# Kernel tuning notes

Measured on AMD Instinct MI355X. Metric: run time of the kernel, lower is better.

## Reference

```python
import jax, jax.numpy as jnp
import numpy as np
from jax import lax

B, H, W, CL, CC, CD, NH, NP = 8, 48, 48, 384, 384, 384, 12, 4
N = H * W
HD = CL // NH
SCALE = HD ** -0.5


def _pool_mat(n, out=7):
    # torch AdaptiveAvgPool2d bin edges: [floor(i*n/out), ceil((i+1)*n/out))
    M = np.zeros((out, n), np.float32)
    for i in range(out):
        s = (i * n) // out
        e = -(-((i + 1) * n) // out)
        M[i, s:e] = 1.0 / (e - s)
    return jnp.asarray(M)


def _resize_mat(out_n, in_n):
    # bilinear, align_corners=False (torch F.interpolate)
    M = np.zeros((out_n, in_n), np.float32)
    scale = in_n / out_n
    for o in range(out_n):
        src = (o + 0.5) * scale - 0.5
        src = min(max(src, 0.0), in_n - 1.0)
        i0 = int(np.floor(src))
        i1 = min(i0 + 1, in_n - 1)
        f = src - i0
        M[o, i0] += 1.0 - f
        M[o, i1] += f
    return jnp.asarray(M)


def _ln_c(x, g, b):
    # LayerNorm over channel dim of NCHW, eps=1e-6
    mu = jnp.mean(x, axis=1, keepdims=True)
    var = jnp.mean((x - mu) ** 2, axis=1, keepdims=True)
    xn = (x - mu) * lax.rsqrt(var + 1e-6)
    return xn * g[None, :, None, None] + b[None, :, None, None]


def _c1(x, w):
    # 1x1 conv, w: (out,in)
    return jnp.einsum('oc,bchw->bohw', w, x)


def _bilerp(feat, grid):
    # feat (G,C,Hs,Ws), grid (G,M,2) xy in [-1,1]; align_corners=False, zero padding
    G, C, Hs, Ws = feat.shape
    x = (grid[..., 0] + 1.0) * 0.5 * Ws - 0.5
    y = (grid[..., 1] + 1.0) * 0.5 * Hs - 0.5
    x0 = jnp.floor(x)
    y0 = jnp.floor(y)
    fx = x - x0
    fy = y - y0
    featf = feat.transpose(0, 2, 3, 1).reshape(G, Hs * Ws, C)
    x0i = x0.astype(jnp.int32)
    y0i = y0.astype(jnp.int32)

    def corner(ix, iy):
        valid = ((ix >= 0) & (ix < Ws) & (iy >= 0) & (iy < Hs)).astype(feat.dtype)
        flat = jnp.clip(iy, 0, Hs - 1) * Ws + jnp.clip(ix, 0, Ws - 1)
        g = jax.vmap(lambda f, i: f[i])(featf, flat)  # (G,M,C)
        return g * valid[..., None]

    v00 = corner(x0i, y0i)
    v01 = corner(x0i + 1, y0i)
    v10 = corner(x0i, y0i + 1)
    v11 = corner(x0i + 1, y0i + 1)
    w00 = ((1 - fx) * (1 - fy))[..., None]
    w01 = (fx * (1 - fy))[..., None]
    w10 = ((1 - fx) * fy)[..., None]
    w11 = (fx * fy)[..., None]
    return v00 * w00 + v01 * w01 + v10 * w10 + v11 * w11  # (G,M,C)


def _forward(local_feat, context_prior, deformable_x, W_q, W_k, W_v, W_pre, ln1_g, ln1_b,
             W_post, dw_w, dw_b, ln2_g, ln2_b, W_lo, b_lo, W_off, b_off,
             attention_biases, W_p, bn_g, bn_b, bn_mean, bn_var):
    q = _c1(local_feat, W_q)  # (B,CL,H,W)

    # context_offset_guide: 1x1 -> GELU -> adaptive pool 7x7 -> LN(C) -> 1x1 to 32 -> resize
    cg = jax.nn.gelu(_c1(context_prior, W_pre), approximate=False)
    Mh, Mw = _pool_mat(H), _pool_mat(W)
    pooled = jnp.einsum('oh,pw,bchw->bcop', Mh, Mw, cg)
    guide = _c1(_ln_c(pooled, ln1_g, ln1_b), W_post)  # (B,32,7,7)
    Uh, Uw = _resize_mat(H, 7), _resize_mat(W, 7)
    guide = jnp.einsum('Oh,Pw,bchw->bcOP', Uh, Uw, guide)  # (B,32,H,W)

    # local_offset_base: dwconv3x3 -> LN(C) -> GELU -> 1x1 to 32
    dw = lax.conv_general_dilated(local_feat, dw_w, (1, 1), [(1, 1), (1, 1)],
                                  dimension_numbers=('NCHW', 'OIHW', 'NCHW'),
                                  feature_group_count=CL) + dw_b[None, :, None, None]
    lo = jax.nn.gelu(_ln_c(dw, ln2_g, ln2_b), approximate=False)
    lo = _c1(lo, W_lo) + b_lo[None, :, None, None]  # (B,32,H,W)

    fused = jnp.concatenate([guide, lo], axis=1)  # (B,64,H,W)
    off = _c1(fused, W_off) + b_off[None, :, None, None]  # (B,NH*NP*2,H,W)
    off = off.transpose(0, 2, 3, 1).reshape(B, H, W, NH, NP, 2)
    offn = off / jnp.asarray([W, H], dtype=off.dtype)

    ry = (jnp.arange(H, dtype=off.dtype) + 0.5) / H
    rx = (jnp.arange(W, dtype=off.dtype) + 0.5) / W
    ref = jnp.stack([jnp.broadcast_to(rx[None, :], (H, W)),
                     jnp.broadcast_to(ry[:, None], (H, W))], axis=-1)  # (H,W,2) xy
    grid = (ref[None, :, :, None, None, :] + offn) * 2.0 - 1.0  # (B,H,W,NH,NP,2)

    gridh = grid.reshape(B, N, NH, NP, 2).transpose(0, 2, 1, 3, 4)  # (B,NH,N,NP,2)
    grid_r = gridh.reshape(B * NH, N * NP, 2)

    k = _c1(context_prior, W_k).reshape(B * NH, HD, H, W)
    v = _c1(deformable_x, W_v).reshape(B * NH, HD, H, W)
    k_s = _bilerp(k, grid_r).reshape(B, NH, N, NP, HD)
    v_s = _bilerp(v, grid_r).reshape(B, NH, N, NP, HD)

    qh = q.reshape(B, NH, HD, N).transpose(0, 1, 3, 2)  # (B,NH,N,HD)
    scores = jnp.einsum('bhnd,bhnpd->bhnp', qh, k_s) * SCALE

    # relative position bias: idx(p1,p2) = |dy|*W + |dx| (first-seen enumeration)
    px = jnp.clip(jnp.round((gridh[..., 0] + 1.0) * 0.5 * W - 0.5), 0, W - 1).astype(jnp.int32)
    py = jnp.clip(jnp.round((gridh[..., 1] + 1.0) * 0.5 * H - 0.5), 0, H - 1).astype(jnp.int32)
    n = jnp.arange(N, dtype=jnp.int32)
    qy = (n // W)[None, None, :, None]
    qx = (n % W)[None, None, :, None]
    bidx = jnp.abs(qy - py) * W + jnp.abs(qx - px)  # (B,NH,N,NP)
    bias = attention_biases[jnp.arange(NH)[None, :, None, None], bidx]

    attn = jax.nn.softmax(scores + bias, axis=-1)
    out = jnp.einsum('bhnp,bhnpd->bhnd', attn, v_s)  # (B,NH,N,HD)
    out = out.transpose(0, 1, 3, 2).reshape(B, CL, H, W)

    y = _c1(out, W_p)
    y = bn_g[None, :, None, None] * (y - bn_mean[None, :, None, None]) * \
        lax.rsqrt(bn_var[None, :, None, None] + 1e-5) + bn_b[None, :, None, None]
    return y


def setup_inputs():
    ks = jax.random.split(jax.random.key(0), 16)
    f32 = jnp.float32
    d = {
        'local_feat': jax.random.normal(ks[0], (B, CL, H, W), f32),
        'context_prior': jax.random.normal(ks[1], (B, CC, H, W), f32),
        'deformable_x': jax.random.normal(ks[2], (B, CD, H, W), f32),
        'W_q': jax.random.normal(ks[3], (CL, CL), f32) * 0.02,
        'W_k': jax.random.normal(ks[4], (CL, CC), f32) * 0.02,
        'W_v': jax.random.normal(ks[5], (CD, CD), f32) * 0.02,
        'W_pre': jax.random.normal(ks[6], (CC, CC), f32) * 0.02,
        'ln1_g': jnp.ones((CC,), f32),
        'ln1_b': jnp.zeros((CC,), f32),
        'W_post': jax.random.normal(ks[7], (32, CC), f32) * 0.02,
        'dw_w': jax.random.normal(ks[8], (CL, 1, 3, 3), f32) * 0.1,
        'dw_b': jnp.zeros((CL,), f32),
        'ln2_g': jnp.ones((CL,), f32),
        'ln2_b': jnp.zeros((CL,), f32),
        'W_lo': jax.random.normal(ks[9], (32, CL), f32) * 0.02,
        'b_lo': jnp.zeros((32,), f32),
        'W_off': jax.random.normal(ks[10], (NH * NP * 2, 64), f32) * 0.01,
        'b_off': jax.random.normal(ks[11], (NH * NP * 2,), f32) * 0.5,
        'attention_biases': jax.random.normal(ks[12], (NH, H * W), f32) * 0.02,
        'W_p': jax.random.normal(ks[13], (CL, CL), f32) * 0.02,
        'bn_g': jnp.ones((CL,), f32),
        'bn_b': jnp.zeros((CL,), f32),
        'bn_mean': jax.random.normal(ks[14], (CL,), f32) * 0.01,
        'bn_var': jax.random.uniform(ks[15], (CL,), f32, 0.5, 1.5),
    }
    return d


def reference(local_feat, context_prior, deformable_x, W_q, W_k, W_v, W_pre, ln1_g, ln1_b,
              W_post, dw_w, dw_b, ln2_g, ln2_b, W_lo, b_lo, W_off, b_off,
              attention_biases, W_p, bn_g, bn_b, bn_mean, bn_var):
    return _forward(local_feat, context_prior, deformable_x, W_q, W_k, W_v, W_pre, ln1_g,
                    ln1_b, W_post, dw_w, dw_b, ln2_g, ln2_b, W_lo, b_lo, W_off, b_off,
                    attention_biases, W_p, bn_g, bn_b, bn_mean, bn_var)
```

## Files before the change

### kernel.cpp

```cpp
#include <hip/hip_runtime.h>
#include <hip/hip_bf16.h>
#include <math.h>

#define B_ 8
#define H_ 48
#define W_ 48
#define N_ 2304
#define C_ 384
#define NH_ 12
#define NP_ 4
#define HD_ 32
#define SCALE_ 0.17677669529663687f

typedef unsigned short ushort;
typedef short bf16x8 __attribute__((ext_vector_type(8)));
typedef float f32x4 __attribute__((ext_vector_type(4)));

__device__ __forceinline__ float b2f(ushort u) {
    union { float f; unsigned i; } x; x.i = ((unsigned)u) << 16; return x.f;
}
__device__ __forceinline__ ushort f2b(float f) {
    __hip_bfloat16 h = __float2bfloat16(f);
    return *(ushort*)&h;
}
__device__ __forceinline__ float geluf(float x) {
    return 0.5f * x * (1.0f + erff(x * 0.70710678118654752440f));
}
__device__ __forceinline__ int iabs(int x) { return x < 0 ? -x : x; }

__device__ __forceinline__ void gl_lds16(const ushort* g, ushort* l) {
    __builtin_amdgcn_global_load_lds(
        (const __attribute__((address_space(1))) unsigned int*)g,
        (__attribute__((address_space(3))) unsigned int*)l, 16, 0, 0);
}

enum { EPI_NONE = 0, EPI_GELU = 1, EPI_BN = 3 };

__global__ void probe_kernel(const void* ones_ptr, int* flag) {
    if (threadIdx.x == 0 && blockIdx.x == 0)
        *flag = (*(const unsigned*)ones_ptr == 0x3F803F80u) ? 1 : 0;
}

#define PREP_MAX 24
struct PrepTab {
    const void* src[PREP_MAX];
    void*       dst[PREP_MAX];
    int         n[PREP_MAX];
    int         tobf[PREP_MAX];
};
__global__ __launch_bounds__(256) void prep_kernel(PrepTab tab, int ne, const int* __restrict__ dflag)
{
    const int isbf = *dflag;
    const int e = blockIdx.y;
    if (e >= ne) return;
    const int n = tab.n[e];
    const void* src = tab.src[e];
    if (tab.tobf[e]) {
        ushort* dst = (ushort*)tab.dst[e];
        if (isbf) {
            const ushort* s = (const ushort*)src;
            for (int i = blockIdx.x * 256 + threadIdx.x; i < n; i += gridDim.x * 256)
                dst[i] = s[i];
        } else {
            const float* s = (const float*)src;
            for (int i = blockIdx.x * 256 + threadIdx.x; i < n; i += gridDim.x * 256)
                dst[i] = f2b(s[i]);
        }
    } else {
        float* dst = (float*)tab.dst[e];
        if (isbf) {
            const ushort* s = (const ushort*)src;
            for (int i = blockIdx.x * 256 + threadIdx.x; i < n; i += gridDim.x * 256)
                dst[i] = b2f(s[i]);
        } else {
            const float* s = (const float*)src;
            for (int i = blockIdx.x * 256 + threadIdx.x; i < n; i += gridDim.x * 256)
                dst[i] = s[i];
        }
    }
}

__global__ void dwt_prep_kernel(const float* __restrict__ WdF, float* __restrict__ WdT)
{
    int c = threadIdx.x;
#pragma unroll
    for (int u = 0; u < 9; u++) WdT[u * C_ + c] = WdF[c * 9 + u];
}

struct TPtrs { const void* src[3]; ushort* dst[3]; };
__global__ __launch_bounds__(256) void transpose3_kernel(TPtrs tp, const int* __restrict__ dflag)
{
    const int isbf = *dflag;
    const int which = blockIdx.z >> 3;
    const int b = blockIdx.z & 7;
    const int n0 = blockIdx.x * 64, c0 = blockIdx.y * 32;
    const void* in = tp.src[which];
    ushort* out = tp.dst[which];
    const int t = threadIdx.x;

    __shared__ unsigned tile[64][33];

    if (isbf) {
        {
            const int c = t >> 3, s = t & 7;
            uint4 v = *(const uint4*)((const ushort*)in + ((size_t)b * C_ + c0 + c) * N_ + n0 + s * 8);
            const int nb = s * 8;
            tile[nb + 0][c] = v.x & 0xffff; tile[nb + 1][c] = v.x >> 16;
            tile[nb + 2][c] = v.y & 0xffff; tile[nb + 3][c] = v.y >> 16;
            tile[nb + 4][c] = v.z & 0xffff; tile[nb + 5][c] = v.z >> 16;
            tile[nb + 6][c] = v.w & 0xffff; tile[nb + 7][c] = v.w >> 16;
        }
        __syncthreads();
        {
            const int n = t >> 2, s = t & 3;
            const int cb = s * 8;
            unsigned p0 = tile[n][cb + 0] | (tile[n][cb + 1] << 16);
            unsigned p1 = tile[n][cb + 2] | (tile[n][cb + 3] << 16);
            unsigned p2 = tile[n][cb + 4] | (tile[n][cb + 5] << 16);
            unsigned p3 = tile[n][cb + 6] | (tile[n][cb + 7] << 16);
            uint4 o; o.x = p0; o.y = p1; o.z = p2; o.w = p3;
            *(uint4*)(out + ((size_t)b * N_ + n0 + n) * C_ + c0 + cb) = o;
        }
    } else {
        float* tf = (float*)&tile[0][0];
        const int tx = t & 31, ty = t >> 5;
        for (int sub = 0; sub < 2; sub++) {
            int ns = n0 + sub * 32;
            __syncthreads();
#pragma unroll
            for (int u = 0; u < 4; u++) {
                int c = ty + u * 8;
                tf[c * 33 + tx] = ((const float*)in)[((size_t)b * C_ + c0 + c) * N_ + ns + tx];
            }
            __syncthreads();
#pragma unroll
            for (int u = 0; u < 4; u++) {
                int n = ty + u * 8;
                out[((size_t)b * N_ + ns + n) * C_ + c0 + tx] = f2b(tf[tx * 33 + n]);
            }
        }
    }
}

template <int EPI, int OUTK>
__global__ __launch_bounds__(256) void gemm_mfma(
    const ushort* __restrict__ Ag, const ushort* __restrict__ Bg, void* __restrict__ Yg,
    int M, int NN, int K, size_t a_bs, size_t b_bs,
    const float* __restrict__ p0, const float* __restrict__ p1,
    const float* __restrict__ p2, const float* __restrict__ p3,
    const int* __restrict__ dflag)
{
    const int isbf = (OUTK == 2) ? *dflag : 1;
    __shared__ ushort As[4][128 * 32];
    __shared__ ushort Bs[4][128 * 32];
    const int tid = threadIdx.x;
    const int m0 = blockIdx.x * 128;
    const int n0 = blockIdx.y * 128;
    const int b  = blockIdx.z;
    const int lane = tid & 63, wave = tid >> 6;
    const int wr = wave >> 1, wc = wave & 1;
    const int quad = lane >> 4, l15 = lane & 15;

    f32x4 acc[4][4];
#pragma unroll
    for (int i = 0; i < 4; i++)
#pragma unroll
        for (int j = 0; j < 4; j++) acc[i][j] = (f32x4){0.f, 0.f, 0.f, 0.f};

    const size_t abase = (size_t)b * a_bs;
    const size_t bbase = (size_t)b * b_bs;
    const int nt = K / 32;

    auto stage = [&](int p, int kc) {
#pragma unroll
        for (int u = 0; u < 2; u++) {
            int idx = tid + 256 * u;
            int r = idx >> 2, s = idx & 3;
            gl_lds16(Ag + abase + (size_t)(m0 + r) * K + kc + 8 * s, &As[p][idx * 8]);
            gl_lds16(Bg + bbase + (size_t)(n0 + r) * K + kc + 8 * s, &Bs[p][idx * 8]);
        }
    };

    stage(0, 0);
    if (nt > 1) stage(1, 32);
    if (nt > 2) stage(2, 64);

    for (int t = 0; t < nt; ++t) {
        if (t + 2 < nt)      asm volatile("s_waitcnt vmcnt(8)" ::: "memory");
        else if (t + 1 < nt) asm volatile("s_waitcnt vmcnt(4)" ::: "memory");
        else                 asm volatile("s_waitcnt vmcnt(0)" ::: "memory");
        __builtin_amdgcn_s_barrier();
        __builtin_amdgcn_sched_barrier(0);
        if (t + 3 < nt) stage((t + 3) & 3, (t + 3) * 32);
        const int p = t & 3;
        bf16x8 af[4], bfr[4];
#pragma unroll
        for (int i = 0; i < 4; i++)
            af[i]  = *(const bf16x8*)&As[p][(wr * 64 + i * 16 + l15) * 32 + quad * 8];
#pragma unroll
        for (int j = 0; j < 4; j++)
            bfr[j] = *(const bf16x8*)&Bs[p][(wc * 64 + j * 16 + l15) * 32 + quad * 8];
#pragma unroll
        for (int i = 0; i < 4; i++)
#pragma unroll
            for (int j = 0; j < 4; j++)
                acc[i][j] = __builtin_amdgcn_mfma_f32_16x16x32_bf16(af[i], bfr[j], acc[i][j], 0, 0, 0);
    }

    const size_t ybase = (size_t)b * (size_t)M * (size_t)NN;
#pragma unroll
    for (int i = 0; i < 4; i++) {
#pragma unroll
        for (int r = 0; r < 4; r++) {
            int m = m0 + wr * 64 + i * 16 + quad * 4 + r;
            float sc = 1.f, sh = 0.f;
            if (EPI == EPI_BN) {
                sc = p0[m] * rsqrtf(p3[m] + 1e-5f);
                sh = p1[m] - sc * p2[m];
            }
#pragma unroll
            for (int j = 0; j < 4; j++) {
                int nn = n0 + wc * 64 + j * 16 + l15;
                float v = acc[i][j][r];
                if (EPI == EPI_GELU) v = geluf(v);
                if (EPI == EPI_BN) v = sc * v + sh;
                size_t yi = ybase + (size_t)m * NN + nn;
                if (OUTK == 0) ((float*)Yg)[yi] = v;
                else if (OUTK == 1) ((ushort*)Yg)[yi] = f2b(v);
                else { if (isbf) ((ushort*)Yg)[yi] = f2b(v); else ((float*)Yg)[yi] = v; }
            }
        }
    }
}

struct QKVPtrs { const ushort* A[3]; const ushort* Bw[3]; ushort* Y[3]; };
__global__ __launch_bounds__(256) void gemm_qkv_kernel(QKVPtrs qp)
{
    const int which = blockIdx.z >> 3;
    const int b = blockIdx.z & 7;
    const ushort* Ag = qp.A[which];
    const ushort* Bg = qp.Bw[which];
    ushort* Yg = qp.Y[which];

    __shared__ ushort As[4][128 * 32];
    __shared__ ushort Bs[4][128 * 32];
    const int tid = threadIdx.x;
    const int m0 = blockIdx.x * 128;
    const int n0 = blockIdx.y * 128;
    const int lane = tid & 63, wave = tid >> 6;
    const int wr = wave >> 1, wc = wave & 1;
    const int quad = lane >> 4, l15 = lane & 15;

    f32x4 acc[4][4];
#pragma unroll
    for (int i = 0; i < 4; i++)
#pragma unroll
        for (int j = 0; j < 4; j++) acc[i][j] = (f32x4){0.f, 0.f, 0.f, 0.f};

    const size_t abase = (size_t)b * (size_t)N_ * C_;

    auto stage = [&](int p, int kc) {
#pragma unroll
        for (int u = 0; u < 2; u++) {
            int idx = tid + 256 * u;
            int r = idx >> 2, s = idx & 3;
            gl_lds16(Ag + abase + (size_t)(m0 + r) * C_ + kc + 8 * s, &As[p][idx * 8]);
            gl_lds16(Bg + (size_t)(n0 + r) * C_ + kc + 8 * s, &Bs[p][idx * 8]);
        }
    };

    stage(0, 0);
    stage(1, 32);
    stage(2, 64);

    const int nt = C_ / 32;
    for (int t = 0; t < nt; ++t) {
        if (t + 2 < nt)      asm volatile("s_waitcnt vmcnt(8)" ::: "memory");
        else if (t + 1 < nt) asm volatile("s_waitcnt vmcnt(4)" ::: "memory");
        else                 asm volatile("s_waitcnt vmcnt(0)" ::: "memory");
        __builtin_amdgcn_s_barrier();
        __builtin_amdgcn_sched_barrier(0);
        if (t + 3 < nt) stage((t + 3) & 3, (t + 3) * 32);
        const int p = t & 3;
        bf16x8 af[4], bfr[4];
#pragma unroll
        for (int i = 0; i < 4; i++)
            af[i]  = *(const bf16x8*)&As[p][(wr * 64 + i * 16 + l15) * 32 + quad * 8];
#pragma unroll
        for (int j = 0; j < 4; j++)
            bfr[j] = *(const bf16x8*)&Bs[p][(wc * 64 + j * 16 + l15) * 32 + quad * 8];
#pragma unroll
        for (int i = 0; i < 4; i++)
#pragma unroll
            for (int j = 0; j < 4; j++)
                acc[i][j] = __builtin_amdgcn_mfma_f32_16x16x32_bf16(af[i], bfr[j], acc[i][j], 0, 0, 0);
    }

    const size_t ybase = abase;
#pragma unroll
    for (int i = 0; i < 4; i++) {
#pragma unroll
        for (int r = 0; r < 4; r++) {
            int m = m0 + wr * 64 + i * 16 + quad * 4 + r;
#pragma unroll
            for (int j = 0; j < 4; j++) {
                int nn = n0 + wc * 64 + j * 16 + l15;
                Yg[ybase + (size_t)m * C_ + nn] = f2b(acc[i][j][r]);
            }
        }
    }
}

__global__ __launch_bounds__(384) void pool_ln_guide_kernel(
    const float* __restrict__ CG, const float* __restrict__ g, const float* __restrict__ bt,
    const ushort* __restrict__ WpostB, float* __restrict__ G7)
{
    const int cell = blockIdx.x % 49, b = blockIdx.x / 49;
    const int i = cell / 7, j = cell % 7, c = threadIdx.x;
    const int sh = (i * H_) / 7, eh = ((i + 1) * H_ + 6) / 7;
    const int sw = (j * W_) / 7, ew = ((j + 1) * W_ + 6) / 7;
    float s = 0.f;
    for (int h = sh; h < eh; h++)
        for (int w = sw; w < ew; w++)
            s += CG[((size_t)b * N_ + h * W_ + w) * C_ + c];
    s *= 1.0f / (float)((eh - sh) * (ew - sw));

    float rs = s, rq = s * s;
#pragma unroll
    for (int m = 1; m <= 32; m <<= 1) {
        rs += __shfl_xor(rs, m);
        rq += __shfl_xor(rq, m);
    }
    __shared__ float ss[6], sq[6], buf[C_];
    __shared__ float psum[12][33];
    int wid = threadIdx.x >> 6;
    if ((threadIdx.x & 63) == 0) { ss[wid] = rs; sq[wid] = rq; }
    __syncthreads();
    if (threadIdx.x == 0) {
        float ts = 0.f, tq = 0.f;
        for (int k = 0; k < 6; k++) { ts += ss[k]; tq += sq[k]; }
        ss[0] = ts; sq[0] = tq;
    }
    __syncthreads();
    float mu = ss[0] / (float)C_;
    float var = sq[0] / (float)C_ - mu * mu;
    float inv = rsqrtf(var + 1e-6f);
    buf[c] = (s - mu) * inv * g[c] + bt[c];
    __syncthreads();

    const int oc = threadIdx.x & 31, seg = threadIdx.x >> 5;
    const uint4* wp = (const uint4*)(WpostB + oc * C_ + seg * 32);
    float part = 0.f;
#pragma unroll
    for (int u = 0; u < 4; u++) {
        uint4 v = wp[u];
        const float* bb = &buf[seg * 32 + u * 8];
        part += b2f((ushort)(v.x & 0xffff)) * bb[0] + b2f((ushort)(v.x >> 16)) * bb[1];
        part += b2f((ushort)(v.y & 0xffff)) * bb[2] + b2f((ushort)(v.y >> 16)) * bb[3];
        part += b2f((ushort)(v.z & 0xffff)) * bb[4] + b2f((ushort)(v.z >> 16)) * bb[5];
        part += b2f((ushort)(v.w & 0xffff)) * bb[6] + b2f((ushort)(v.w >> 16)) * bb[7];
    }
    psum[seg][oc] = part;
    __syncthreads();
    if (threadIdx.x < 32) {
        float acc = 0.f;
#pragma unroll
        for (int k = 0; k < 12; k++) acc += psum[k][threadIdx.x];
        G7[((size_t)b * 49 + cell) * 32 + threadIdx.x] = acc;
    }
}

__global__ __launch_bounds__(384) void wcomb_prep_kernel(
    const ushort* __restrict__ WoffB, const ushort* __restrict__ WloB,
    const float* __restrict__ bloF, const float* __restrict__ boffF,
    ushort* __restrict__ Bext, float* __restrict__ biasp)
{
    const int co = blockIdx.x;
    const int c = threadIdx.x;
    float acc = 0.f;
#pragma unroll 8
    for (int j = 0; j < 32; j++)
        acc += b2f(WoffB[co * 64 + 32 + j]) * b2f(WloB[j * 384 + c]);
    ushort hi = f2b(acc);
    float r = acc - b2f(hi);
    ushort lo = f2b(r);
    Bext[co * 1152 + c] = hi;
    Bext[co * 1152 + 384 + c] = lo;
    Bext[co * 1152 + 768 + c] = hi;
    if (c == 0) {
        float bp = boffF[co];
        for (int j = 0; j < 32; j++)
            bp += b2f(WoffB[co * 64 + 32 + j]) * bloF[j];
        biasp[co] = bp;
    }
}

__global__ void og7_prep_kernel(
    const ushort* __restrict__ WoffB, const float* __restrict__ G7, float* __restrict__ OG7)
{
    const int bc = blockIdx.x;
    const int co = threadIdx.x;
    if (co >= 96) return;
    const float* g = G7 + (size_t)bc * 32;
    float acc = 0.f;
#pragma unroll 8
    for (int c = 0; c < 32; c++)
        acc += b2f(WoffB[co * 64 + c]) * g[c];
    OG7[(size_t)bc * 96 + co] = acc;
}

__global__ __launch_bounds__(512) void dw_ln_gelu_kernel(
    const ushort* __restrict__ LF, const float* __restrict__ WdT, const float* __restrict__ BdF,
    const float* __restrict__ g, const float* __restrict__ bt,
    ushort* __restrict__ AHI, ushort* __restrict__ ALO)
{
    const int wave = threadIdx.x >> 6, lane = threadIdx.x & 63;
    const int m = blockIdx.x * 8 + wave;
    const int b = m / N_, n = m % N_;
    const int h = n / W_, w = n % W_;
    const bool act = lane < 48;
    const int c0 = lane * 8;

    float acc[8];
#pragma unroll
    for (int j = 0; j < 8; j++) acc[j] = 0.f;
    if (act) {
        f32x4 b0 = *(const f32x4*)(BdF + c0);
        f32x4 b1 = *(const f32x4*)(BdF + c0 + 4);
#pragma unroll
        for (int j = 0; j < 4; j++) { acc[j] = b0[j]; acc[4 + j] = b1[j]; }
    }

#pragma unroll
    for (int u = 0; u < 9; u++) {
        const int ky = u / 3, kx = u % 3;
        const int y = h + ky - 1, x = w + kx - 1;
        if (act && y >= 0 && y < H_ && x >= 0 && x < W_) {
            uint4 v = *(const uint4*)(LF + ((size_t)b * N_ + y * W_ + x) * C_ + c0);
            f32x4 wa = *(const f32x4*)(WdT + u * C_ + c0);
            f32x4 wb = *(const f32x4*)(WdT + u * C_ + c0 + 4);
            acc[0] += wa[0] * b2f((ushort)(v.x & 0xffff));
            acc[1] += wa[1] * b2f((ushort)(v.x >> 16));
            acc[2] += wa[2] * b2f((ushort)(v.y & 0xffff));
            acc[3] += wa[3] * b2f((ushort)(v.y >> 16));
            acc[4] += wb[0] * b2f((ushort)(v.z & 0xffff));
            acc[5] += wb[1] * b2f((ushort)(v.z >> 16));
            acc[6] += wb[2] * b2f((ushort)(v.w & 0xffff));
            acc[7] += wb[3] * b2f((ushort)(v.w >> 16));
        }
    }

    float rs = 0.f, rq = 0.f;
#pragma unroll
    for (int j = 0; j < 8; j++) { rs += acc[j]; rq += acc[j] * acc[j]; }
#pragma unroll
    for (int s = 1; s <= 32; s <<= 1) {
        rs += __shfl_xor(rs, s);
        rq += __shfl_xor(rq, s);
    }
    float mu = rs / (float)C_;
    float var = rq / (float)C_ - mu * mu;
    float inv = rsqrtf(var + 1e-6f);

    if (act) {
        f32x4 g0 = *(const f32x4*)(g + c0);
        f32x4 g1 = *(const f32x4*)(g + c0 + 4);
        f32x4 t0 = *(const f32x4*)(bt + c0);
        f32x4 t1 = *(const f32x4*)(bt + c0 + 4);
        float v[8];
#pragma unroll
        for (int j = 0; j < 4; j++) {
            v[j]     = geluf((acc[j]     - mu) * inv * g0[j] + t0[j]);
            v[4 + j] = geluf((acc[4 + j] - mu) * inv * g1[j] + t1[j]);
        }
        uint4 hi, lo;
        ushort hs[8], ls[8];
#pragma unroll
        for (int j = 0; j < 8; j++) {
            hs[j] = f2b(v[j]);
            ls[j] = f2b(v[j] - b2f(hs[j]));
        }
        hi.x = (unsigned)hs[0] | ((unsigned)hs[1] << 16);
        hi.y = (unsigned)hs[2] | ((unsigned)hs[3] << 16);
        hi.z = (unsigned)hs[4] | ((unsigned)hs[5] << 16);
        hi.w = (unsigned)hs[6] | ((unsigned)hs[7] << 16);
        lo.x = (unsigned)ls[0] | ((unsigned)ls[1] << 16);
        lo.y = (unsigned)ls[2] | ((unsigned)ls[3] << 16);
        lo.z = (unsigned)ls[4] | ((unsigned)ls[5] << 16);
        lo.w = (unsigned)ls[6] | ((unsigned)ls[7] << 16);
        size_t idx = (size_t)m * C_ + c0;
        *(uint4*)(AHI + idx) = hi;
        *(uint4*)(ALO + idx) = lo;
    }
}

__global__ __launch_bounds__(256) void off_gemm_kernel(
    const ushort* __restrict__ AHI, const ushort* __restrict__ ALO,
    const ushort* __restrict__ Bext, float* __restrict__ OFFP)
{
    __shared__ ushort As[4][128 * 32];
    __shared__ ushort Bs[4][128 * 32];
    const int tid = threadIdx.x;
    const int m0 = blockIdx.x * 128;
    const int seg = blockIdx.y;
    const ushort* Ag = (seg < 2) ? AHI : ALO;
    const int bcol0 = seg * 384;
    const int lane = tid & 63, wave = tid >> 6;
    const int wr = wave >> 1, wc = wave & 1;
    const int quad = lane >> 4, l15 = lane & 15;

    f32x4 acc[4][3];
#pragma unroll
    for (int i = 0; i < 4; i++)
#pragma unroll
        for (int j = 0; j < 3; j++) acc[i][j] = (f32x4){0.f, 0.f, 0.f, 0.f};

    auto stage = [&](int p, int kc) {
#pragma unroll
        for (int u = 0; u < 2; u++) {
            int idx = tid + 256 * u;
            int r = idx >> 2, s = idx & 3;
            int rb = r < 96 ? r : 95;
            gl_lds16(Ag + (size_t)(m0 + r) * 384 + kc + 8 * s, &As[p][idx * 8]);
            gl_lds16(Bext + (size_t)rb * 1152 + bcol0 + kc + 8 * s, &Bs[p][idx * 8]);
        }
    };

    stage(0, 0);
    stage(1, 32);
    stage(2, 64);

    const int nt = 12;
    for (int t = 0; t < nt; ++t) {
        if (t + 2 < nt)      asm volatile("s_waitcnt vmcnt(8)" ::: "memory");
        else if (t + 1 < nt) asm volatile("s_waitcnt vmcnt(4)" ::: "memory");
        else                 asm volatile("s_waitcnt vmcnt(0)" ::: "memory");
        __builtin_amdgcn_s_barrier();
        __builtin_amdgcn_sched_barrier(0);
        if (t + 3 < nt) stage((t + 3) & 3, (t + 3) * 32);
        const int p = t & 3;
        bf16x8 af[4], bfr[3];
#pragma unroll
        for (int i = 0; i < 4; i++)
            af[i]  = *(const bf16x8*)&As[p][(wr * 64 + i * 16 + l15) * 32 + quad * 8];
#pragma unroll
        for (int j = 0; j < 3; j++)
            bfr[j] = *(const bf16x8*)&Bs[p][(wc * 48 + j * 16 + l15) * 32 + quad * 8];
#pragma unroll
        for (int i = 0; i < 4; i++)
#pragma unroll
            for (int j = 0; j < 3; j++)
                acc[i][j] = __builtin_amdgcn_mfma_f32_16x16x32_bf16(af[i], bfr[j], acc[i][j], 0, 0, 0);
    }

    float* out = OFFP + (size_t)seg * ((size_t)B_ * N_ * 96);
#pragma unroll
    for (int i = 0; i < 4; i++) {
#pragma unroll
        for (int r = 0; r < 4; r++) {
            int m = m0 + wr * 64 + i * 16 + quad * 4 + r;
#pragma unroll
            for (int j = 0; j < 3; j++) {
                int co = wc * 48 + j * 16 + l15;
                out[(size_t)m * 96 + co] = acc[i][j][r];
            }
        }
    }
}

__global__ __launch_bounds__(384) void attn_kernel(
    const ushort* __restrict__ Q, const ushort* __restrict__ K, const ushort* __restrict__ V,
    const float* __restrict__ OFFP, const float* __restrict__ biasp,
    const float* __restrict__ OG7,
    const float* __restrict__ ABf, ushort* __restrict__ OUT)
{
    const int pairi = blockIdx.x;
    const int b = pairi / (N_ / 2);
    const int n0 = (pairi % (N_ / 2)) * 2;
    const int tid = threadIdx.x;

    __shared__ int   cidxS[96][4];
    __shared__ float cwS[96][4];
    __shared__ float biasS[96];

    if (tid < 96) {
        const int pos = tid / 48, idx = tid % 48;
        const int n = n0 + pos;
        const int h = n / W_, w = n % W_;
        const int nh = idx >> 2, p = idx & 3;
        const int co = nh * 8 + 2 * p;

        const float fs = 7.0f / 48.0f;
        float sy = fminf(fmaxf(((float)h + 0.5f) * fs - 0.5f, 0.f), 6.f);
        float sx = fminf(fmaxf(((float)w + 0.5f) * fs - 0.5f, 0.f), 6.f);
        int gy0 = (int)floorf(sy), gx0 = (int)floorf(sx);
        int gy1 = min(gy0 + 1, 6), gx1 = min(gx0 + 1, 6);
        float gfy = sy - (float)gy0, gfx = sx - (float)gx0;
        float bw00 = (1.f - gfy) * (1.f - gfx), bw01 = (1.f - gfy) * gfx;
        float bw10 = gfy * (1.f - gfx), bw11 = gfy * gfx;
        const float* ogb = OG7 + (size_t)b * 49 * 96;
        int c00 = (gy0 * 7 + gx0) * 96, c01 = (gy0 * 7 + gx1) * 96;
        int c10 = (gy1 * 7 + gx0) * 96, c11 = (gy1 * 7 + gx1) * 96;
        const size_t MS = (size_t)B_ * N_ * 96;
        const size_t mrow = ((size_t)b * N_ + n) * 96;

        float ox = OFFP[mrow + co] + OFFP[MS + mrow + co] + OFFP[2 * MS + mrow + co]
                 + biasp[co]
                 + bw00 * ogb[c00 + co] + bw01 * ogb[c01 + co]
                 + bw10 * ogb[c10 + co] + bw11 * ogb[c11 + co];
        float oy = OFFP[mrow + co + 1] + OFFP[MS + mrow + co + 1] + OFFP[2 * MS + mrow + co + 1]
                 + biasp[co + 1]
                 + bw00 * ogb[c00 + co + 1] + bw01 * ogb[c01 + co + 1]
                 + bw10 * ogb[c10 + co + 1] + bw11 * ogb[c11 + co + 1];

        float x = (float)w + ox;
        float y = (float)h + oy;

        int px = (int)fminf(fmaxf(rintf(x), 0.f), (float)(W_ - 1));
        int py = (int)fminf(fmaxf(rintf(y), 0.f), (float)(H_ - 1));
        biasS[tid] = ABf[(size_t)nh * N_ + iabs(h - py) * W_ + iabs(w - px)];

        float x0f = floorf(x), y0f = floorf(y);
        float fx = x - x0f, fy = y - y0f;
        int x0 = (int)x0f, y0 = (int)y0f;
#pragma unroll
        for (int cc = 0; cc < 4; cc++) {
            int dx = cc & 1, dy = cc >> 1;
            int ix = x0 + dx, iy = y0 + dy;
            bool valid = (ix >= 0) && (ix < W_) && (iy >= 0) && (iy < H_);
            int ixc = min(max(ix, 0), W_ - 1), iyc = min(max(iy, 0), H_ - 1);
            cidxS[tid][cc] = iyc * W_ + ixc;
            float wx = dx ? fx : (1.f - fx);
            float wy = dy ? fy : (1.f - fy);
            cwS[tid][cc] = valid ? wx * wy : 0.f;
        }
    }
    __syncthreads();

    const int pos = tid / 192, r = tid % 192;
    const int nh = r >> 4, dd = r & 15;
    const int n = n0 + pos;
    const size_t row = ((size_t)b * N_ + n) * C_ + nh * HD_ + dd * 2;
    unsigned qu = *(const unsigned*)(Q + row);
    const float q0 = b2f((ushort)(qu & 0xffff));
    const float q1 = b2f((ushort)(qu >> 16));
    const size_t kvbase = (size_t)b * N_ * C_ + nh * HD_ + dd * 2;
    const int s0 = pos * 48 + nh * 4;

    int   ci[NP_][4];
    float cw[NP_][4];
#pragma unroll
    for (int p = 0; p < NP_; p++)
#pragma unroll
        for (int cc = 0; cc < 4; cc++) {
            ci[p][cc] = cidxS[s0 + p][cc];
            cw[p][cc] = cwS[s0 + p][cc];
        }

    float sc[NP_];
#pragma unroll
    for (int p = 0; p < NP_; p++) {
        float ks0 = 0.f, ks1 = 0.f;
#pragma unroll
        for (int cc = 0; cc < 4; cc++) {
            unsigned kv = *(const unsigned*)(K + kvbase + (size_t)ci[p][cc] * C_);
            ks0 += cw[p][cc] * b2f((ushort)(kv & 0xffff));
            ks1 += cw[p][cc] * b2f((ushort)(kv >> 16));
        }
        float dot = q0 * ks0 + q1 * ks1;
#pragma unroll
        for (int m = 1; m <= 8; m <<= 1) dot += __shfl_xor(dot, m);
        sc[p] = dot * SCALE_ + biasS[s0 + p];
    }

    float m = fmaxf(fmaxf(sc[0], sc[1]), fmaxf(sc[2], sc[3]));
    float e[NP_], esum = 0.f;
#pragma unroll
    for (int p = 0; p < NP_; p++) { e[p] = __expf(sc[p] - m); esum += e[p]; }
    float inv = 1.0f / esum;

    float o0 = 0.f, o1 = 0.f;
#pragma unroll
    for (int p = 0; p < NP_; p++) {
        float vs0 = 0.f, vs1 = 0.f;
#pragma unroll
        for (int cc = 0; cc < 4; cc++) {
            unsigned vv = *(const unsigned*)(V + kvbase + (size_t)ci[p][cc] * C_);
            vs0 += cw[p][cc] * b2f((ushort)(vv & 0xffff));
            vs1 += cw[p][cc] * b2f((ushort)(vv >> 16));
        }
        float ep = e[p] * inv;
        o0 += ep * vs0;
        o1 += ep * vs1;
    }
    unsigned ou = (unsigned)f2b(o0) | ((unsigned)f2b(o1) << 16);
    *(unsigned*)(OUT + row) = ou;
}

extern "C" void kernel_launch(void* const* d_in, const int* in_sizes, int n_in,
                              void* d_out, int out_size, void* d_ws, size_t ws_size,
                              hipStream_t stream)
{
    const void* local_feat    = d_in[0];
    const void* context_prior = d_in[1];
    const void* deformable_x  = d_in[2];

    const size_t BIGE = (size_t)B_ * N_ * C_;

    char* wsb = (char*)d_ws;
    auto carve = [&](size_t bytes) { char* p = wsb; wsb += (bytes + 255) & ~(size_t)255; return p; };
    int*    flag = (int*)carve(256);
    ushort* T1   = (ushort*)carve(BIGE * 2);
    ushort* T2   = (ushort*)carve(BIGE * 2);
    ushort* T3   = (ushort*)carve(BIGE * 2);
    ushort* Qb   = (ushort*)carve(BIGE * 2);
    ushort* Kb   = (ushort*)carve(BIGE * 2);
    float*  CGR  = (float*)carve(BIGE * 4);
    float*  OFFB = (float*)carve((size_t)B_ * N_ * 96 * 4 * 3);
    float*  G7   = (float*)carve((size_t)B_ * 49 * 32 * 4);
    ushort* WqB   = (ushort*)carve(147456 * 2);
    ushort* WkB   = (ushort*)carve(147456 * 2);
    ushort* WvB   = (ushort*)carve(147456 * 2);
    ushort* WpreB = (ushort*)carve(147456 * 2);
    ushort* WpB   = (ushort*)carve(147456 * 2);
    ushort* WpostB= (ushort*)carve(12288 * 2);
    ushort* WloB  = (ushort*)carve(12288 * 2);
    ushort* WoffB = (ushort*)carve(6144 * 2);
    ushort* Bext  = (ushort*)carve(96 * 1152 * 2);
    float*  biasp = (float*)carve(96 * 4);
    float*  OG7   = (float*)carve((size_t)B_ * 49 * 96 * 4);
    float*  dwwF  = (float*)carve(3456 * 4);
    float*  dwwT  = (float*)carve(3456 * 4);
    float*  ABf   = (float*)carve(27648 * 4);
    float*  bloF  = (float*)carve(32 * 4);
    float*  boffF = (float*)carve(96 * 4);
    float*  dwbF  = (float*)carve(384 * 4);
    float*  ln1gF = (float*)carve(384 * 4);
    float*  ln1bF = (float*)carve(384 * 4);
    float*  ln2gF = (float*)carve(384 * 4);
    float*  ln2bF = (float*)carve(384 * 4);
    float*  bngF  = (float*)carve(384 * 4);
    float*  bnbF  = (float*)carve(384 * 4);
    float*  bnmF  = (float*)carve(384 * 4);
    float*  bnvF  = (float*)carve(384 * 4);
    ushort* Vb   = (ushort*)CGR;
    ushort* AOut = (ushort*)CGR + BIGE;
    ushort* AHI  = Qb;
    ushort* ALO  = Kb;

    probe_kernel<<<1, 64, 0, stream>>>(d_in[7] , flag);

    PrepTab tab;
    int ne = 0;
    auto add = [&](const void* s, void* d, int n, int tb) {
        tab.src[ne] = s; tab.dst[ne] = d; tab.n[ne] = n; tab.tobf[ne] = tb; ne++;
    };
    add(d_in[3],  WqB,   147456, 1);
    add(d_in[4],  WkB,   147456, 1);
    add(d_in[5],  WvB,   147456, 1);
    add(d_in[6],  WpreB, 147456, 1);
    add(d_in[19], WpB,   147456, 1);
    add(d_in[9],  WpostB, 12288, 1);
    add(d_in[14], WloB,   12288, 1);
    add(d_in[16], WoffB,   6144, 1);
    add(d_in[10], dwwF,    3456, 0);
    add(d_in[18], ABf,    27648, 0);
    add(d_in[15], bloF,      32, 0);
    add(d_in[17], boffF,     96, 0);
    add(d_in[11], dwbF,     384, 0);
    add(d_in[7],  ln1gF,    384, 0);
    add(d_in[8],  ln1bF,    384, 0);
    add(d_in[12], ln2gF,    384, 0);
    add(d_in[13], ln2bF,    384, 0);
    add(d_in[20], bngF,     384, 0);
    add(d_in[21], bnbF,     384, 0);
    add(d_in[22], bnmF,     384, 0);
    add(d_in[23], bnvF,     384, 0);
    prep_kernel<<<dim3(64, ne), 256, 0, stream>>>(tab, ne, flag);
    dwt_prep_kernel<<<1, 384, 0, stream>>>(dwwF, dwwT);

    dim3 blk256(256);
    dim3 t3grid(N_ / 64, C_ / 32, 3 * B_);
    dim3 ggrid(N_ / 128, C_ / 128, B_);
    dim3 qkvgrid(N_ / 128, C_ / 128, 3 * B_);
    dim3 fgrid(C_ / 128, N_ / 128, B_);
    dim3 offgrid((B_ * N_) / 128, 3);
    const size_t BST = (size_t)N_ * C_;

    TPtrs tp;
    tp.src[0] = local_feat;    tp.dst[0] = T1;
    tp.src[1] = context_prior; tp.dst[1] = T2;
    tp.src[2] = deformable_x;  tp.dst[2] = T3;
    transpose3_kernel<<<t3grid, blk256, 0, stream>>>(tp, flag);

    wcomb_prep_kernel<<<96, 384, 0, stream>>>(WoffB, WloB, bloF, boffF, Bext, biasp);

    gemm_mfma<EPI_GELU, 0><<<ggrid, blk256, 0, stream>>>(
        T2, WpreB, CGR, N_, C_, C_, BST, 0, nullptr, nullptr, nullptr, nullptr, flag);
    pool_ln_guide_kernel<<<B_ * 49, 384, 0, stream>>>(CGR, ln1gF, ln1bF, WpostB, G7);
    og7_prep_kernel<<<B_ * 49, 96, 0, stream>>>(WoffB, G7, OG7);

    dw_ln_gelu_kernel<<<(B_ * N_) / 8, 512, 0, stream>>>(T1, dwwT, dwbF, ln2gF, ln2bF, AHI, ALO);

    off_gemm_kernel<<<offgrid, blk256, 0, stream>>>(AHI, ALO, Bext, OFFB);

    QKVPtrs qp;
    qp.A[0] = T1; qp.Bw[0] = WqB; qp.Y[0] = Qb;
    qp.A[1] = T2; qp.Bw[1] = WkB; qp.Y[1] = Kb;
    qp.A[2] = T3; qp.Bw[2] = WvB; qp.Y[2] = Vb;
    gemm_qkv_kernel<<<qkvgrid, blk256, 0, stream>>>(qp);

    attn_kernel<<<(B_ * N_) / 2, 384, 0, stream>>>(Qb, Kb, Vb, OFFB, biasp, OG7, ABf, AOut);

    gemm_mfma<EPI_BN, 2><<<fgrid, blk256, 0, stream>>>(
        WpB, AOut, d_out, C_, N_, C_, 0, BST, bngF, bnbF, bnmF, bnvF, flag);
}
```

Baseline: 359.7 us.

## Merge pre-GEMM into batched QKV launch and split-K the final projection

Folds the W_pre GELU GEMM into the batched QKV kernel as a fourth grid slice, shrinks the LDS pipeline from four stages to double buffering with launch bounds requesting more resident blocks, and reorders launches. The final projection GEMM becomes split-K over two halves that write fp32 partials into reused transpose buffers, followed by a separate combine kernel that applies BatchNorm and the output cast. The aim is fewer launches, higher occupancy and more blocks for the small final GEMM. The cost is extra fp32 partial traffic and one more kernel, plus a shallower prefetch pipeline and buffers that are no longer aliased.

```diff
diff --git a/kernel.cpp b/kernel.cpp
--- a/kernel.cpp
+++ b/kernel.cpp
@@ -33,8 +33,6 @@
         (const __attribute__((address_space(1))) unsigned int*)g,
         (__attribute__((address_space(3))) unsigned int*)l, 16, 0, 0);
 }
-
-enum { EPI_NONE = 0, EPI_GELU = 1, EPI_BN = 3 };
 
 __global__ void probe_kernel(const void* ones_ptr, int* flag) {
     if (threadIdx.x == 0 && blockIdx.x == 0)
@@ -142,108 +140,16 @@
     }
 }
 
-template <int EPI, int OUTK>
-__global__ __launch_bounds__(256) void gemm_mfma(
-    const ushort* __restrict__ Ag, const ushort* __restrict__ Bg, void* __restrict__ Yg,
-    int M, int NN, int K, size_t a_bs, size_t b_bs,
-    const float* __restrict__ p0, const float* __restrict__ p1,
-    const float* __restrict__ p2, const float* __restrict__ p3,
-    const int* __restrict__ dflag)
-{
-    const int isbf = (OUTK == 2) ? *dflag : 1;
-    __shared__ ushort As[4][128 * 32];
-    __shared__ ushort Bs[4][128 * 32];
-    const int tid = threadIdx.x;
-    const int m0 = blockIdx.x * 128;
-    const int n0 = blockIdx.y * 128;
-    const int b  = blockIdx.z;
-    const int lane = tid & 63, wave = tid >> 6;
-    const int wr = wave >> 1, wc = wave & 1;
-    const int quad = lane >> 4, l15 = lane & 15;
-
-    f32x4 acc[4][4];
-#pragma unroll
-    for (int i = 0; i < 4; i++)
-#pragma unroll
-        for (int j = 0; j < 4; j++) acc[i][j] = (f32x4){0.f, 0.f, 0.f, 0.f};
-
-    const size_t abase = (size_t)b * a_bs;
-    const size_t bbase = (size_t)b * b_bs;
-    const int nt = K / 32;
-
-    auto stage = [&](int p, int kc) {
-#pragma unroll
-        for (int u = 0; u < 2; u++) {
-            int idx = tid + 256 * u;
-            int r = idx >> 2, s = idx & 3;
-            gl_lds16(Ag + abase + (size_t)(m0 + r) * K + kc + 8 * s, &As[p][idx * 8]);
-            gl_lds16(Bg + bbase + (size_t)(n0 + r) * K + kc + 8 * s, &Bs[p][idx * 8]);
-        }
-    };
-
-    stage(0, 0);
-    if (nt > 1) stage(1, 32);
-    if (nt > 2) stage(2, 64);
-
-    for (int t = 0; t < nt; ++t) {
-        if (t + 2 < nt)      asm volatile("s_waitcnt vmcnt(8)" ::: "memory");
-        else if (t + 1 < nt) asm volatile("s_waitcnt vmcnt(4)" ::: "memory");
-        else                 asm volatile("s_waitcnt vmcnt(0)" ::: "memory");
-        __builtin_amdgcn_s_barrier();
-        __builtin_amdgcn_sched_barrier(0);
-        if (t + 3 < nt) stage((t + 3) & 3, (t + 3) * 32);
-        const int p = t & 3;
-        bf16x8 af[4], bfr[4];
-#pragma unroll
-        for (int i = 0; i < 4; i++)
-            af[i]  = *(const bf16x8*)&As[p][(wr * 64 + i * 16 + l15) * 32 + quad * 8];
-#pragma unroll
-        for (int j = 0; j < 4; j++)
-            bfr[j] = *(const bf16x8*)&Bs[p][(wc * 64 + j * 16 + l15) * 32 + quad * 8];
-#pragma unroll
-        for (int i = 0; i < 4; i++)
-#pragma unroll
-            for (int j = 0; j < 4; j++)
-                acc[i][j] = __builtin_amdgcn_mfma_f32_16x16x32_bf16(af[i], bfr[j], acc[i][j], 0, 0, 0);
-    }
-
-    const size_t ybase = (size_t)b * (size_t)M * (size_t)NN;
-#pragma unroll
-    for (int i = 0; i < 4; i++) {
-#pragma unroll
-        for (int r = 0; r < 4; r++) {
-            int m = m0 + wr * 64 + i * 16 + quad * 4 + r;
-            float sc = 1.f, sh = 0.f;
-            if (EPI == EPI_BN) {
-                sc = p0[m] * rsqrtf(p3[m] + 1e-5f);
-                sh = p1[m] - sc * p2[m];
-            }
-#pragma unroll
-            for (int j = 0; j < 4; j++) {
-                int nn = n0 + wc * 64 + j * 16 + l15;
-                float v = acc[i][j][r];
-                if (EPI == EPI_GELU) v = geluf(v);
-                if (EPI == EPI_BN) v = sc * v + sh;
-                size_t yi = ybase + (size_t)m * NN + nn;
-                if (OUTK == 0) ((float*)Yg)[yi] = v;
-                else if (OUTK == 1) ((ushort*)Yg)[yi] = f2b(v);
-                else { if (isbf) ((ushort*)Yg)[yi] = f2b(v); else ((float*)Yg)[yi] = v; }
-            }
-        }
-    }
-}
-
-struct QKVPtrs { const ushort* A[3]; const ushort* Bw[3]; ushort* Y[3]; };
-__global__ __launch_bounds__(256) void gemm_qkv_kernel(QKVPtrs qp)
+struct QKV4Ptrs { const ushort* A[4]; const ushort* Bw[4]; void* Y[4]; };
+__global__ __launch_bounds__(256, 5) void gemm_qkv4_kernel(QKV4Ptrs qp)
 {
     const int which = blockIdx.z >> 3;
     const int b = blockIdx.z & 7;
     const ushort* Ag = qp.A[which];
     const ushort* Bg = qp.Bw[which];
-    ushort* Yg = qp.Y[which];
-
-    __shared__ ushort As[4][128 * 32];
-    __shared__ ushort Bs[4][128 * 32];
+
+    __shared__ ushort As[2][128 * 32];
+    __shared__ ushort Bs[2][128 * 32];
     const int tid = threadIdx.x;
     const int m0 = blockIdx.x * 128;
     const int n0 = blockIdx.y * 128;
@@ -270,18 +176,18 @@
     };
 
     stage(0, 0);
-    stage(1, 32);
-    stage(2, 64);
 
     const int nt = C_ / 32;
     for (int t = 0; t < nt; ++t) {
-        if (t + 2 < nt)      asm volatile("s_waitcnt vmcnt(8)" ::: "memory");
-        else if (t + 1 < nt) asm volatile("s_waitcnt vmcnt(4)" ::: "memory");
-        else                 asm volatile("s_waitcnt vmcnt(0)" ::: "memory");
+        if (t + 1 < nt) {
+            stage((t + 1) & 1, (t + 1) * 32);
+            asm volatile("s_waitcnt vmcnt(4)" ::: "memory");
+        } else {
+            asm volatile("s_waitcnt vmcnt(0)" ::: "memory");
+        }
         __builtin_amdgcn_s_barrier();
         __builtin_amdgcn_sched_barrier(0);
-        if (t + 3 < nt) stage((t + 3) & 3, (t + 3) * 32);
-        const int p = t & 3;
+        const int p = t & 1;
         bf16x8 af[4], bfr[4];
 #pragma unroll
         for (int i = 0; i < 4; i++)
@@ -294,9 +200,104 @@
 #pragma unroll
             for (int j = 0; j < 4; j++)
                 acc[i][j] = __builtin_amdgcn_mfma_f32_16x16x32_bf16(af[i], bfr[j], acc[i][j], 0, 0, 0);
-    }
-
-    const size_t ybase = abase;
+        __builtin_amdgcn_s_barrier();
+    }
+
+    if (which < 3) {
+        ushort* Yg = (ushort*)qp.Y[which];
+#pragma unroll
+        for (int i = 0; i < 4; i++) {
+#pragma unroll
+            for (int r = 0; r < 4; r++) {
+                int m = m0 + wr * 64 + i * 16 + quad * 4 + r;
+#pragma unroll
+                for (int j = 0; j < 4; j++) {
+                    int nn = n0 + wc * 64 + j * 16 + l15;
+                    Yg[abase + (size_t)m * C_ + nn] = f2b(acc[i][j][r]);
+                }
+            }
+        }
+    } else {
+        float* Yg = (float*)qp.Y[3];
+#pragma unroll
+        for (int i = 0; i < 4; i++) {
+#pragma unroll
+            for (int r = 0; r < 4; r++) {
+                int m = m0 + wr * 64 + i * 16 + quad * 4 + r;
+#pragma unroll
+                for (int j = 0; j < 4; j++) {
+                    int nn = n0 + wc * 64 + j * 16 + l15;
+                    Yg[abase + (size_t)m * C_ + nn] = geluf(acc[i][j][r]);
+                }
+            }
+        }
+    }
+}
+
+__global__ __launch_bounds__(256) void gemm_final_splitk(
+    const ushort* __restrict__ WpB, const ushort* __restrict__ AOut,
+    float* __restrict__ PF0, float* __restrict__ PF1)
+{
+    const int b  = blockIdx.z >> 1;
+    const int ks = blockIdx.z & 1;
+    const int kc0 = ks * 192;
+
+    __shared__ ushort As[2][128 * 32];
+    __shared__ ushort Bs[2][128 * 32];
+    const int tid = threadIdx.x;
+    const int m0 = blockIdx.x * 128;
+    const int n0 = blockIdx.y * 128;
+    const int lane = tid & 63, wave = tid >> 6;
+    const int wr = wave >> 1, wc = wave & 1;
+    const int quad = lane >> 4, l15 = lane & 15;
+
+    f32x4 acc[4][4];
+#pragma unroll
+    for (int i = 0; i < 4; i++)
+#pragma unroll
+        for (int j = 0; j < 4; j++) acc[i][j] = (f32x4){0.f, 0.f, 0.f, 0.f};
+
+    const size_t bbase = (size_t)b * (size_t)N_ * C_;
+
+    auto stage = [&](int p, int kc) {
+#pragma unroll
+        for (int u = 0; u < 2; u++) {
+            int idx = tid + 256 * u;
+            int r = idx >> 2, s = idx & 3;
+            gl_lds16(WpB + (size_t)(m0 + r) * C_ + kc0 + kc + 8 * s, &As[p][idx * 8]);
+            gl_lds16(AOut + bbase + (size_t)(n0 + r) * C_ + kc0 + kc + 8 * s, &Bs[p][idx * 8]);
+        }
+    };
+
+    stage(0, 0);
+
+    const int nt = 6;
+    for (int t = 0; t < nt; ++t) {
+        if (t + 1 < nt) {
+            stage((t + 1) & 1, (t + 1) * 32);
+            asm volatile("s_waitcnt vmcnt(4)" ::: "memory");
+        } else {
+            asm volatile("s_waitcnt vmcnt(0)" ::: "memory");
+        }
+        __builtin_amdgcn_s_barrier();
+        __builtin_amdgcn_sched_barrier(0);
+        const int p = t & 1;
+        bf16x8 af[4], bfr[4];
+#pragma unroll
+        for (int i = 0; i < 4; i++)
+            af[i]  = *(const bf16x8*)&As[p][(wr * 64 + i * 16 + l15) * 32 + quad * 8];
+#pragma unroll
+        for (int j = 0; j < 4; j++)
+            bfr[j] = *(const bf16x8*)&Bs[p][(wc * 64 + j * 16 + l15) * 32 + quad * 8];
+#pragma unroll
+        for (int i = 0; i < 4; i++)
+#pragma unroll
+            for (int j = 0; j < 4; j++)
+                acc[i][j] = __builtin_amdgcn_mfma_f32_16x16x32_bf16(af[i], bfr[j], acc[i][j], 0, 0, 0);
+        __builtin_amdgcn_s_barrier();
+    }
+
+    float* out = (ks == 0 ? PF0 : PF1) + (size_t)b * (size_t)C_ * N_;
 #pragma unroll
     for (int i = 0; i < 4; i++) {
 #pragma unroll
@@ -305,8 +306,37 @@
 #pragma unroll
             for (int j = 0; j < 4; j++) {
                 int nn = n0 + wc * 64 + j * 16 + l15;
-                Yg[ybase + (size_t)m * C_ + nn] = f2b(acc[i][j][r]);
+                out[(size_t)m * N_ + nn] = acc[i][j][r];
             }
+        }
+    }
+}
+
+__global__ __launch_bounds__(256) void combine_bn_kernel(
+    const float* __restrict__ PF0, const float* __restrict__ PF1,
+    void* __restrict__ Yg,
+    const float* __restrict__ bng, const float* __restrict__ bnb,
+    const float* __restrict__ bnm, const float* __restrict__ bnv,
+    const int* __restrict__ dflag)
+{
+    const int isbf = *dflag;
+    const size_t nv4 = (size_t)B_ * C_ * N_ / 4;
+    for (size_t i = blockIdx.x * 256 + threadIdx.x; i < nv4; i += (size_t)gridDim.x * 256) {
+        const size_t e0 = i * 4;
+        const int co = (int)((e0 / N_) % C_);
+        float sc = bng[co] * rsqrtf(bnv[co] + 1e-5f);
+        float sh = bnb[co] - sc * bnm[co];
+        f32x4 a = *(const f32x4*)(PF0 + e0);
+        f32x4 b = *(const f32x4*)(PF1 + e0);
+        f32x4 v;
+#pragma unroll
+        for (int j = 0; j < 4; j++) v[j] = sc * (a[j] + b[j]) + sh;
+        if (isbf) {
+            ushort4 o;
+            o.x = f2b(v[0]); o.y = f2b(v[1]); o.z = f2b(v[2]); o.w = f2b(v[3]);
+            *(ushort4*)((ushort*)Yg + e0) = o;
+        } else {
+            *(f32x4*)((float*)Yg + e0) = v;
         }
     }
 }
@@ -715,6 +745,9 @@
     ushort* T3   = (ushort*)carve(BIGE * 2);
     ushort* Qb   = (ushort*)carve(BIGE * 2);
     ushort* Kb   = (ushort*)carve(BIGE * 2);
+    ushort* Vb   = (ushort*)carve(BIGE * 2);
+    ushort* AHI  = (ushort*)carve(BIGE * 2);
+    ushort* ALO  = (ushort*)carve(BIGE * 2);
     float*  CGR  = (float*)carve(BIGE * 4);
     float*  OFFB = (float*)carve((size_t)B_ * N_ * 96 * 4 * 3);
     float*  G7   = (float*)carve((size_t)B_ * 49 * 32 * 4);
@@ -743,10 +776,9 @@
     float*  bnbF  = (float*)carve(384 * 4);
     float*  bnmF  = (float*)carve(384 * 4);
     float*  bnvF  = (float*)carve(384 * 4);
-    ushort* Vb   = (ushort*)CGR;
     ushort* AOut = (ushort*)CGR + BIGE;
-    ushort* AHI  = Qb;
-    ushort* ALO  = Kb;
+    float*  PF0  = (float*)T1;
+    float*  PF1  = (float*)T3;
 
     probe_kernel<<<1, 64, 0, stream>>>(d_in[7] , flag);
 
@@ -781,11 +813,9 @@
 
     dim3 blk256(256);
     dim3 t3grid(N_ / 64, C_ / 32, 3 * B_);
-    dim3 ggrid(N_ / 128, C_ / 128, B_);
-    dim3 qkvgrid(N_ / 128, C_ / 128, 3 * B_);
-    dim3 fgrid(C_ / 128, N_ / 128, B_);
+    dim3 qkv4grid(N_ / 128, C_ / 128, 4 * B_);
     dim3 offgrid((B_ * N_) / 128, 3);
-    const size_t BST = (size_t)N_ * C_;
+    dim3 fingrid(C_ / 128, N_ / 128, 2 * B_);
 
     TPtrs tp;
     tp.src[0] = local_feat;    tp.dst[0] = T1;
@@ -795,23 +825,23 @@
 
     wcomb_prep_kernel<<<96, 384, 0, stream>>>(WoffB, WloB, bloF, boffF, Bext, biasp);
 
-    gemm_mfma<EPI_GELU, 0><<<ggrid, blk256, 0, stream>>>(
-        T2, WpreB, CGR, N_, C_, C_, BST, 0, nullptr, nullptr, nullptr, nullptr, flag);
+    dw_ln_gelu_kernel<<<(B_ * N_) / 8, 512, 0, stream>>>(T1, dwwT, dwbF, ln2gF, ln2bF, AHI, ALO);
+
+    off_gemm_kernel<<<offgrid, blk256, 0, stream>>>(AHI, ALO, Bext, OFFB);
+
+    QKV4Ptrs qp;
+    qp.A[0] = T1; qp.Bw[0] = WqB;   qp.Y[0] = Qb;
+    qp.A[1] = T2; qp.Bw[1] = WkB;   qp.Y[1] = Kb;
+    qp.A[2] = T3; qp.Bw[2] = WvB;   qp.Y[2] = Vb;
+    qp.A[3] = T2; qp.Bw[3] = WpreB; qp.Y[3] = CGR;
+    gemm_qkv4_kernel<<<qkv4grid, blk256, 0, stream>>>(qp);
+
     pool_ln_guide_kernel<<<B_ * 49, 384, 0, stream>>>(CGR, ln1gF, ln1bF, WpostB, G7);
     og7_prep_kernel<<<B_ * 49, 96, 0, stream>>>(WoffB, G7, OG7);
 
-    dw_ln_gelu_kernel<<<(B_ * N_) / 8, 512, 0, stream>>>(T1, dwwT, dwbF, ln2gF, ln2bF, AHI, ALO);
-
-    off_gemm_kernel<<<offgrid, blk256, 0, stream>>>(AHI, ALO, Bext, OFFB);
-
-    QKVPtrs qp;
-    qp.A[0] = T1; qp.Bw[0] = WqB; qp.Y[0] = Qb;
-    qp.A[1] = T2; qp.Bw[1] = WkB; qp.Y[1] = Kb;
-    qp.A[2] = T3; qp.Bw[2] = WvB; qp.Y[2] = Vb;
-    gemm_qkv_kernel<<<qkvgrid, blk256, 0, stream>>>(qp);
-
     attn_kernel<<<(B_ * N_) / 2, 384, 0, stream>>>(Qb, Kb, Vb, OFFB, biasp, OG7, ABf, AOut);
 
-    gemm_mfma<EPI_BN, 2><<<fgrid, blk256, 0, stream>>>(
-        WpB, AOut, d_out, C_, N_, C_, 0, BST, bngF, bnbF, bnmF, bnvF, flag);
-}
+    gemm_final_splitk<<<fingrid, blk256, 0, stream>>>(WpB, AOut, PF0, PF1);
+
+    combine_bn_kernel<<<2048, blk256, 0, stream>>>(PF0, PF1, d_out, bngF, bnbF, bnmF, bnvF, flag);
+}
```

Result: no change. 357.1 us (-0.7%).
